# Kernel optimization log

Measured on AMD Instinct MI355X. Metric: run time of the kernel, lower is better.

Reference implementation:

```python
import jax, jax.numpy as jnp
import numpy as np

# ---- structural constants (mirror e3nn SO3.tensor_productRs bookkeeping) ----
MUL = 2                      # multiplicity of every irrep in Rs_in / Rs_out
LS = [0, 1, 2]               # irrep orders present in Rs_in and Rs_out
L_MAX = 2                    # spherical-harmonics cutoff -> Y_dim = 9
N_BASIS, HIDDEN = 64, 64     # radial model sizes
R_MAX, GAMMA = 3.5, 4.0      # gaussian radial basis params


def _filter_paths():
    """One entry (l_filter) per (mul_out, mul_in, l_in, l_out, l_f) path."""
    paths = []
    for l_in in LS:
        for l_out in LS:
            for lf in range(abs(l_in - l_out), min(l_in + l_out, L_MAX) + 1):
                paths.extend([lf] * (MUL * MUL))  # mul_in * mul_out copies
    return paths  # len == n_path == 60


def _build_mix_matrices():
    """rf_mix[K, n_path]: broadcast each radial path weight over its 2l+1 components.
    ylm_mix[K, 9]: select Y_{l,m} for each filter component. Both 0/1, block sparse."""
    paths = _filter_paths()
    n_path = len(paths)
    K = sum(2 * l + 1 for l in paths)          # 204
    y_off = {0: 0, 1: 1, 2: 4}                 # offset of l-block inside Y (dim 9)
    rf = np.zeros((K, n_path), dtype=np.float32)
    ylm = np.zeros((K, 9), dtype=np.float32)
    k = 0
    for p, l in enumerate(paths):
        for m in range(2 * l + 1):
            rf[k, p] = 1.0
            ylm[k, y_off[l] + m] = 1.0
            k += 1
    return rf, ylm, n_path, K


def _sh_l012(n):
    """Real spherical harmonics l=0..2 on unit vectors n[Z,3] -> Y[9, Z]."""
    x, y, z = n[:, 0], n[:, 1], n[:, 2]
    c0 = 0.28209479177387814   # 1/(2 sqrt(pi))
    c1 = 0.4886025119029199    # sqrt(3/(4 pi))
    c2a = 1.0925484305920792   # sqrt(15/(4 pi))
    c2b = 0.31539156525252005  # sqrt(5/(16 pi))
    c2c = 0.5462742152960396   # sqrt(15/(16 pi))
    one = jnp.ones_like(x)
    return jnp.stack([
        c0 * one,
        c1 * y, c1 * z, c1 * x,
        c2a * x * y, c2a * y * z, c2b * (3.0 * z * z - 1.0), c2a * x * z,
        c2c * (x * x - y * y),
    ], axis=0)


def setup_inputs() -> dict:
    key = jax.random.key(0)
    k_r, k_cg, k_w1, k_w2 = jax.random.split(key, 4)
    Z = 65536
    D = MUL * sum(2 * l + 1 for l in LS)       # 18 (dim_in == dim_out)
    rf_np, ylm_np, n_path, K = _build_mix_matrices()
    r = 2.0 * jax.random.normal(k_r, (Z, 3), dtype=jnp.float32)
    cg = jax.random.normal(k_cg, (K, D, D), dtype=jnp.float32) / np.sqrt(K)
    W1 = jax.random.normal(k_w1, (N_BASIS, HIDDEN), dtype=jnp.float32) / np.sqrt(N_BASIS)
    b1 = jnp.zeros((HIDDEN,), dtype=jnp.float32)
    W2 = jax.random.normal(k_w2, (HIDDEN, n_path), dtype=jnp.float32) / np.sqrt(HIDDEN)
    b2 = jnp.zeros((n_path,), dtype=jnp.float32)
    return {"r": r, "W1": W1, "b1": b1, "W2": W2, "b2": b2,
            "cg": cg, "rf_mix": jnp.asarray(rf_np), "ylm_mix": jnp.asarray(ylm_np)}


def reference(r, W1, b1, W2, b2, cg, rf_mix, ylm_mix):
    radii = jnp.linalg.norm(r, axis=1)                    # [Z]
    n = r / (radii[:, None] + 1e-12)                      # unit directions
    Y = _sh_l012(n)                                       # [9, Z]  (sh returns [m, ...])
    centers = jnp.linspace(0.0, R_MAX, N_BASIS, dtype=jnp.float32)
    B = jnp.exp(-GAMMA * (radii[:, None] - centers) ** 2) # gaussian radial basis [Z, 64]
    R = jax.nn.relu(B @ W1 + b1) @ W2 + b2                # RadialModel -> [Z, n_path]
    Rm = jnp.einsum('kp,zp->zk', rf_mix, R)               # 'ij,zj->zi'
    Ym = jnp.einsum('ky,yz->zk', ylm_mix, Y)              # 'ij,jz->zi'
    # 'kij,zk,zk->zij' : fuse the two per-point vectors, then one GEMM over k
    kernel = jnp.einsum('kij,zk->zij', cg, Rm * Ym)       # [Z, 18, 18]
    return kernel
```

## Files before the change

kernel.cpp:

```cpp
#include <hip/hip_runtime.h>

#define NPATH 60
#define KDIM  204
#define KPAD  224
#define NIJ   324
#define NTIL  21
#define HID   64

typedef short bf16x8 __attribute__((ext_vector_type(8)));
typedef float f32x4  __attribute__((ext_vector_type(4)));

__device__ __align__(16) unsigned short g_w1s[4096];
__device__ __align__(16) unsigned short g_w2s[4096];
__device__ __align__(16) unsigned short g_cgs[75264];
__device__ unsigned char g_ptab[KDIM];
__device__ unsigned char g_ytab[KDIM];

__device__ inline unsigned short f2bf(float f) {
    unsigned int u = __builtin_bit_cast(unsigned int, f);
    u += 0x7fffu + ((u >> 16) & 1u);
    return (unsigned short)(u >> 16);
}
__device__ inline float bf2f(unsigned short h) {
    unsigned int u = ((unsigned int)h) << 16;
    return __builtin_bit_cast(float, u);
}

__global__ void prep_kernel(const float* __restrict__ W1, const float* __restrict__ W2,
                            const float* __restrict__ cg, const float* __restrict__ rf,
                            const float* __restrict__ ylm)
{
    int idx = blockIdx.x * 256 + threadIdx.x;
    if (idx < 4096) {
        int e = idx & 7, ln = (idx >> 3) & 63, nt = (idx >> 9) & 3, kc = idx >> 11;
        int k = kc * 32 + (ln >> 4) * 8 + e;
        int n = nt * 16 + (ln & 15);
        g_w1s[idx] = f2bf(W1[k * HID + n]);
    } else if (idx < 8192) {
        int j = idx - 4096;
        int e = j & 7, ln = (j >> 3) & 63, nt = (j >> 9) & 3, kc = j >> 11;
        int k = kc * 32 + (ln >> 4) * 8 + e;
        int n = nt * 16 + (ln & 15);
        g_w2s[j] = f2bf(n < NPATH ? W2[k * NPATH + n] : 0.0f);
    } else if (idx < 8192 + 75264) {
        int j = idx - 8192;
        int e = j & 7, ln = (j >> 3) & 63;
        int nt = (j >> 9) % NTIL;
        int kc = j / (512 * NTIL);
        int k = kc * 32 + (ln >> 4) * 8 + e;
        int n = nt * 16 + (ln & 15);
        g_cgs[j] = f2bf((k < KDIM && n < NIJ) ? cg[k * NIJ + n] : 0.0f);
    } else if (idx < 8192 + 75264 + KDIM) {
        int k = idx - (8192 + 75264);
        int p = 0, yy = 0;
        for (int q = 0; q < NPATH; q++) if (rf[k * NPATH + q] != 0.0f) p = q;
        for (int q = 0; q < 9; q++)     if (ylm[k * 9 + q]   != 0.0f) yy = q;
        g_ptab[k] = (unsigned char)p;
        g_ytab[k] = (unsigned char)yy;
    }
}

union SmemU {
    struct {
        unsigned short Blds[64][72];
        unsigned short Hlds[64][72];
    } p1;
    unsigned short Clds[64][228];
    float stage[16][340];
};

__global__ __launch_bounds__(256) void fused_kernel(
    const float* __restrict__ r, const float* __restrict__ b1,
    const float* __restrict__ b2, float* __restrict__ out)
{
    __shared__ SmemU sm;
    __shared__ unsigned short Rl[64][61];
    __shared__ float Yl[64][9];
    __shared__ float radl[64];
    __shared__ unsigned char ptabL[KDIM];
    __shared__ unsigned char ytabL[KDIM];

    const int tid  = threadIdx.x;
    const int wv   = tid >> 6;
    const int lane = tid & 63;
    const int quad = lane >> 4;
    const int l16  = lane & 15;
    const int z0   = blockIdx.x * 64;

    if (tid < 64) {
        int z = z0 + tid;
        float x = r[z * 3 + 0], y = r[z * 3 + 1], zc = r[z * 3 + 2];
        float rad = sqrtf(x * x + y * y + zc * zc);
        float inv = 1.0f / (rad + 1e-12f);
        float nx = x * inv, ny = y * inv, nz = zc * inv;
        radl[tid] = rad;
        const float c0 = 0.28209479177387814f, c1 = 0.4886025119029199f;
        const float c2a = 1.0925484305920792f, c2b = 0.31539156525252005f, c2c = 0.5462742152960396f;
        Yl[tid][0] = c0;
        Yl[tid][1] = c1 * ny;
        Yl[tid][2] = c1 * nz;
        Yl[tid][3] = c1 * nx;
        Yl[tid][4] = c2a * nx * ny;
        Yl[tid][5] = c2a * ny * nz;
        Yl[tid][6] = c2b * (3.0f * nz * nz - 1.0f);
        Yl[tid][7] = c2a * nx * nz;
        Yl[tid][8] = c2c * (nx * nx - ny * ny);
    }
    for (int k = tid; k < KDIM; k += 256) {
        ptabL[k] = g_ptab[k];
        ytabL[k] = g_ytab[k];
    }
    __syncthreads();

    {
        int zz = tid >> 2, grp = tid & 3;
        float rad = radl[zz];
        unsigned int* dst = (unsigned int*)&sm.p1.Blds[zz][grp * 16];
        const float step = 3.5f / 63.0f;
        #pragma unroll
        for (int ii = 0; ii < 8; ii++) {
            int i0 = grp * 16 + ii * 2;
            float d0 = rad - (float)i0 * step;
            float d1 = rad - (float)(i0 + 1) * step;
            unsigned int u0 = f2bf(expf(-4.0f * d0 * d0));
            unsigned int u1 = f2bf(expf(-4.0f * d1 * d1));
            dst[ii] = u0 | (u1 << 16);
        }
    }
    __syncthreads();

    {
        bf16x8 a0 = *(const bf16x8*)&sm.p1.Blds[wv * 16 + l16][0 + quad * 8];
        bf16x8 a1 = *(const bf16x8*)&sm.p1.Blds[wv * 16 + l16][32 + quad * 8];
        #pragma unroll
        for (int nt = 0; nt < 4; nt++) {
            bf16x8 bb0 = *(const bf16x8*)&g_w1s[((0 * 4 + nt) * 64 + lane) * 8];
            bf16x8 bb1 = *(const bf16x8*)&g_w1s[((1 * 4 + nt) * 64 + lane) * 8];
            f32x4 acc = {0.f, 0.f, 0.f, 0.f};
            acc = __builtin_amdgcn_mfma_f32_16x16x32_bf16(a0, bb0, acc, 0, 0, 0);
            acc = __builtin_amdgcn_mfma_f32_16x16x32_bf16(a1, bb1, acc, 0, 0, 0);
            int h = nt * 16 + l16;
            float bias = b1[h];
            #pragma unroll
            for (int rr = 0; rr < 4; rr++) {
                float v = acc[rr] + bias;
                v = v > 0.0f ? v : 0.0f;
                sm.p1.Hlds[wv * 16 + quad * 4 + rr][h] = f2bf(v);
            }
        }
    }
    __syncthreads();

    {
        bf16x8 a0 = *(const bf16x8*)&sm.p1.Hlds[wv * 16 + l16][0 + quad * 8];
        bf16x8 a1 = *(const bf16x8*)&sm.p1.Hlds[wv * 16 + l16][32 + quad * 8];
        #pragma unroll
        for (int nt = 0; nt < 4; nt++) {
            bf16x8 bb0 = *(const bf16x8*)&g_w2s[((0 * 4 + nt) * 64 + lane) * 8];
            bf16x8 bb1 = *(const bf16x8*)&g_w2s[((1 * 4 + nt) * 64 + lane) * 8];
            f32x4 acc = {0.f, 0.f, 0.f, 0.f};
            acc = __builtin_amdgcn_mfma_f32_16x16x32_bf16(a0, bb0, acc, 0, 0, 0);
            acc = __builtin_amdgcn_mfma_f32_16x16x32_bf16(a1, bb1, acc, 0, 0, 0);
            int p = nt * 16 + l16;
            if (p < NPATH) {
                float bias = b2[p];
                #pragma unroll
                for (int rr = 0; rr < 4; rr++)
                    Rl[wv * 16 + quad * 4 + rr][p] = f2bf(acc[rr] + bias);
            }
        }
    }
    __syncthreads();

    for (int idx = tid; idx < 64 * (KPAD / 2); idx += 256) {
        int z = idx / (KPAD / 2);
        int k = (idx % (KPAD / 2)) * 2;
        unsigned int u = 0;
        if (k < KDIM) {
            float cA = bf2f(Rl[z][ptabL[k]])     * Yl[z][ytabL[k]];
            float cB = bf2f(Rl[z][ptabL[k + 1]]) * Yl[z][ytabL[k + 1]];
            u = (unsigned int)f2bf(cA) | ((unsigned int)f2bf(cB) << 16);
        }
        *(unsigned int*)&sm.Clds[z][k] = u;
    }
    __syncthreads();

    const int ntb = wv * 5 + (wv > 0 ? 1 : 0);
    const int cnt = (wv == 0) ? 6 : 5;

    f32x4 acc[6][4];
    #pragma unroll
    for (int i = 0; i < 6; i++)
        #pragma unroll
        for (int zt = 0; zt < 4; zt++)
            acc[i][zt] = (f32x4){0.f, 0.f, 0.f, 0.f};

    #pragma unroll
    for (int kc = 0; kc < 7; kc++) {
        bf16x8 az[4];
        #pragma unroll
        for (int zt = 0; zt < 4; zt++)
            az[zt] = *(const bf16x8*)&sm.Clds[zt * 16 + l16][kc * 32 + quad * 8];

        bf16x8 bg[6];
        #pragma unroll
        for (int i = 0; i < 6; i++) {
            int nt = ntb + i; if (nt > NTIL - 1) nt = NTIL - 1;
            bg[i] = *(const bf16x8*)&g_cgs[((kc * NTIL + nt) * 64 + lane) * 8];
        }
        #pragma unroll
        for (int i = 0; i < 6; i++) {
            if (i < cnt) {
                #pragma unroll
                for (int zt = 0; zt < 4; zt++)
                    acc[i][zt] = __builtin_amdgcn_mfma_f32_16x16x32_bf16(az[zt], bg[i], acc[i][zt], 0, 0, 0);
            }
        }
    }

    for (int zt = 0; zt < 4; zt++) {
        __syncthreads();
        #pragma unroll
        for (int i = 0; i < 6; i++) {
            if (i < cnt) {
                int col = (ntb + i) * 16 + l16;
                #pragma unroll
                for (int rr = 0; rr < 4; rr++)
                    sm.stage[quad * 4 + rr][col] = acc[i][zt][rr];
            }
        }
        __syncthreads();
        for (int j = tid; j < 16 * (NIJ / 4); j += 256) {
            int row = j / (NIJ / 4);
            int c4  = j % (NIJ / 4);
            f32x4 v = *(const f32x4*)&sm.stage[row][c4 * 4];
            *(f32x4*)&out[(z0 + zt * 16 + row) * NIJ + c4 * 4] = v;
        }
    }
}

extern "C" void kernel_launch(void* const* d_in, const int* in_sizes, int n_in,
                              void* d_out, int out_size, void* d_ws, size_t ws_size,
                              hipStream_t stream) {
    const float* r   = (const float*)d_in[0];
    const float* W1  = (const float*)d_in[1];
    const float* b1  = (const float*)d_in[2];
    const float* W2  = (const float*)d_in[3];
    const float* b2  = (const float*)d_in[4];
    const float* cg  = (const float*)d_in[5];
    const float* rf  = (const float*)d_in[6];
    const float* ylm = (const float*)d_in[7];
    float* out = (float*)d_out;

    const int Z = in_sizes[0] / 3;

    prep_kernel<<<327, 256, 0, stream>>>(W1, W2, cg, rf, ylm);
    fused_kernel<<<Z / 64, 256, 0, stream>>>(r, b1, b2, out);
}
```

Measured before the change: 138.9 us.

## Split fused kernel into coefficient kernel and streaming GEMM kernel via workspace

Splits the single fused kernel in two. The first computes per-point bf16 coefficients in MFMA fragment layout and writes them to a global workspace. The second reads those fragments and runs the CG GEMM over 128 points per block, storing fp32 results straight to global without LDS staging. This drops the large staging buffer and several barriers and rebalances the tile shape. In exchange it adds a global round trip of the coefficients, an extra launch, and uncoalesced scalar output stores with a stride of NIJ.

```diff
diff --git a/kernel.cpp b/kernel.cpp
--- a/kernel.cpp
+++ b/kernel.cpp
@@ -60,23 +60,22 @@
     }
 }
 
+
 union SmemU {
     struct {
         unsigned short Blds[64][72];
         unsigned short Hlds[64][72];
     } p1;
     unsigned short Clds[64][228];
-    float stage[16][340];
 };
 
-__global__ __launch_bounds__(256) void fused_kernel(
+__global__ __launch_bounds__(256) void coeff_kernel(
     const float* __restrict__ r, const float* __restrict__ b1,
-    const float* __restrict__ b2, float* __restrict__ out)
+    const float* __restrict__ b2, unsigned short* __restrict__ coeff_f)
 {
     __shared__ SmemU sm;
     __shared__ unsigned short Rl[64][61];
     __shared__ float Yl[64][9];
-    __shared__ float radl[64];
     __shared__ unsigned char ptabL[KDIM];
     __shared__ unsigned char ytabL[KDIM];
 
@@ -93,7 +92,6 @@
         float rad = sqrtf(x * x + y * y + zc * zc);
         float inv = 1.0f / (rad + 1e-12f);
         float nx = x * inv, ny = y * inv, nz = zc * inv;
-        radl[tid] = rad;
         const float c0 = 0.28209479177387814f, c1 = 0.4886025119029199f;
         const float c2a = 1.0925484305920792f, c2b = 0.31539156525252005f, c2c = 0.5462742152960396f;
         Yl[tid][0] = c0;
@@ -110,11 +108,12 @@
         ptabL[k] = g_ptab[k];
         ytabL[k] = g_ytab[k];
     }
-    __syncthreads();
 
     {
         int zz = tid >> 2, grp = tid & 3;
-        float rad = radl[zz];
+        int z = z0 + zz;
+        float x = r[z * 3 + 0], y = r[z * 3 + 1], zc = r[z * 3 + 2];
+        float rad = sqrtf(x * x + y * y + zc * zc);
         unsigned int* dst = (unsigned int*)&sm.p1.Blds[zz][grp * 16];
         const float step = 3.5f / 63.0f;
         #pragma unroll
@@ -185,56 +184,67 @@
     }
     __syncthreads();
 
-    const int ntb = wv * 5 + (wv > 0 ? 1 : 0);
-    const int cnt = (wv == 0) ? 6 : 5;
-
-    f32x4 acc[6][4];
+    {
+        const long ztg = blockIdx.x * 4 + wv;
+        #pragma unroll
+        for (int kc = 0; kc < 7; kc++) {
+            bf16x8 v = *(const bf16x8*)&sm.Clds[wv * 16 + l16][kc * 32 + quad * 8];
+            *(bf16x8*)&coeff_f[((ztg * 7 + kc) * 64 + lane) * 8] = v;
+        }
+    }
+}
+
+__global__ __launch_bounds__(256) void gemm_kernel(
+    const unsigned short* __restrict__ coeff_f, float* __restrict__ out)
+{
+    const int tid  = threadIdx.x;
+    const int wv   = tid >> 6;
+    const int lane = tid & 63;
+    const int quad = lane >> 4;
+    const int l16  = lane & 15;
+    const int z0   = blockIdx.x * 128;
+    const long ztg0 = (long)(z0 >> 4) + wv * 2;
+
     #pragma unroll
-    for (int i = 0; i < 6; i++)
-        #pragma unroll
-        for (int zt = 0; zt < 4; zt++)
-            acc[i][zt] = (f32x4){0.f, 0.f, 0.f, 0.f};
-
-    #pragma unroll
-    for (int kc = 0; kc < 7; kc++) {
-        bf16x8 az[4];
-        #pragma unroll
-        for (int zt = 0; zt < 4; zt++)
-            az[zt] = *(const bf16x8*)&sm.Clds[zt * 16 + l16][kc * 32 + quad * 8];
-
-        bf16x8 bg[6];
+    for (int chunk = 0; chunk < 4; chunk++) {
+        const int ntb = (chunk == 0) ? 0 : (1 + chunk * 5);
+        const int cnt = (chunk == 0) ? 6 : 5;
+
+        f32x4 acc[6][2];
         #pragma unroll
         for (int i = 0; i < 6; i++) {
-            int nt = ntb + i; if (nt > NTIL - 1) nt = NTIL - 1;
-            bg[i] = *(const bf16x8*)&g_cgs[((kc * NTIL + nt) * 64 + lane) * 8];
-        }
-        #pragma unroll
-        for (int i = 0; i < 6; i++) {
-            if (i < cnt) {
-                #pragma unroll
-                for (int zt = 0; zt < 4; zt++)
-                    acc[i][zt] = __builtin_amdgcn_mfma_f32_16x16x32_bf16(az[zt], bg[i], acc[i][zt], 0, 0, 0);
-            }
-        }
-    }
-
-    for (int zt = 0; zt < 4; zt++) {
-        __syncthreads();
+            acc[i][0] = (f32x4){0.f, 0.f, 0.f, 0.f};
+            acc[i][1] = (f32x4){0.f, 0.f, 0.f, 0.f};
+        }
+
+        #pragma unroll
+        for (int kc = 0; kc < 7; kc++) {
+            bf16x8 az0 = *(const bf16x8*)&coeff_f[((ztg0 * 7 + kc) * 64 + lane) * 8];
+            bf16x8 az1 = *(const bf16x8*)&coeff_f[(((ztg0 + 1) * 7 + kc) * 64 + lane) * 8];
+            #pragma unroll
+            for (int i = 0; i < 6; i++) {
+                if (i < cnt) {
+                    bf16x8 bg = *(const bf16x8*)&g_cgs[((kc * NTIL + ntb + i) * 64 + lane) * 8];
+                    acc[i][0] = __builtin_amdgcn_mfma_f32_16x16x32_bf16(az0, bg, acc[i][0], 0, 0, 0);
+                    acc[i][1] = __builtin_amdgcn_mfma_f32_16x16x32_bf16(az1, bg, acc[i][1], 0, 0, 0);
+                }
+            }
+        }
+
         #pragma unroll
         for (int i = 0; i < 6; i++) {
             if (i < cnt) {
                 int col = (ntb + i) * 16 + l16;
-                #pragma unroll
-                for (int rr = 0; rr < 4; rr++)
-                    sm.stage[quad * 4 + rr][col] = acc[i][zt][rr];
-            }
-        }
-        __syncthreads();
-        for (int j = tid; j < 16 * (NIJ / 4); j += 256) {
-            int row = j / (NIJ / 4);
-            int c4  = j % (NIJ / 4);
-            f32x4 v = *(const f32x4*)&sm.stage[row][c4 * 4];
-            *(f32x4*)&out[(z0 + zt * 16 + row) * NIJ + c4 * 4] = v;
+                if (col < NIJ) {
+                    #pragma unroll
+                    for (int t = 0; t < 2; t++) {
+                        int zb = z0 + (wv * 2 + t) * 16 + quad * 4;
+                        #pragma unroll
+                        for (int rr = 0; rr < 4; rr++)
+                            out[(long)(zb + rr) * NIJ + col] = acc[i][t][rr];
+                    }
+                }
+            }
         }
     }
 }
@@ -253,7 +263,9 @@
     float* out = (float*)d_out;
 
     const int Z = in_sizes[0] / 3;
+    unsigned short* coeff_f = (unsigned short*)d_ws;
 
     prep_kernel<<<327, 256, 0, stream>>>(W1, W2, cg, rf, ylm);
-    fused_kernel<<<Z / 64, 256, 0, stream>>>(r, b1, b2, out);
-}
+    coeff_kernel<<<Z / 64, 256, 0, stream>>>(r, b1, b2, coeff_f);
+    gemm_kernel<<<Z / 128, 256, 0, stream>>>(coeff_f, out);
+}
```

New measurement: 169.1 us. 21.8% more time.

## Swap MFMA operands to store output directly from registers, drop LDS staging

Applied to the files above, without the earlier changes.

The GEMM operands are swapped so each lane's accumulator holds four consecutive output columns for a single point. The results can then be written to global memory as float4 stores without the shared-memory staging buffer and its per-tile barriers. The radius is recomputed per thread instead of being shared through LDS, which removes one barrier. Each row is now written in 16-byte pieces scattered across rows instead of fully coalesced rows. The smaller shared-memory footprint may also allow higher occupancy.

```diff
diff --git a/kernel.cpp b/kernel.cpp
--- a/kernel.cpp
+++ b/kernel.cpp
@@ -66,7 +66,6 @@
         unsigned short Hlds[64][72];
     } p1;
     unsigned short Clds[64][228];
-    float stage[16][340];
 };
 
 __global__ __launch_bounds__(256) void fused_kernel(
@@ -76,7 +75,6 @@
     __shared__ SmemU sm;
     __shared__ unsigned short Rl[64][61];
     __shared__ float Yl[64][9];
-    __shared__ float radl[64];
     __shared__ unsigned char ptabL[KDIM];
     __shared__ unsigned char ytabL[KDIM];
 
@@ -93,7 +91,6 @@
         float rad = sqrtf(x * x + y * y + zc * zc);
         float inv = 1.0f / (rad + 1e-12f);
         float nx = x * inv, ny = y * inv, nz = zc * inv;
-        radl[tid] = rad;
         const float c0 = 0.28209479177387814f, c1 = 0.4886025119029199f;
         const float c2a = 1.0925484305920792f, c2b = 0.31539156525252005f, c2c = 0.5462742152960396f;
         Yl[tid][0] = c0;
@@ -110,11 +107,11 @@
         ptabL[k] = g_ptab[k];
         ytabL[k] = g_ytab[k];
     }
-    __syncthreads();
-
     {
         int zz = tid >> 2, grp = tid & 3;
-        float rad = radl[zz];
+        int z = z0 + zz;
+        float x = r[z * 3 + 0], y = r[z * 3 + 1], zc = r[z * 3 + 2];
+        float rad = sqrtf(x * x + y * y + zc * zc);
         unsigned int* dst = (unsigned int*)&sm.p1.Blds[zz][grp * 16];
         const float step = 3.5f / 63.0f;
         #pragma unroll
@@ -185,56 +182,47 @@
     }
     __syncthreads();
 
-    const int ntb = wv * 5 + (wv > 0 ? 1 : 0);
-    const int cnt = (wv == 0) ? 6 : 5;
-
-    f32x4 acc[6][4];
-    #pragma unroll
-    for (int i = 0; i < 6; i++)
-        #pragma unroll
-        for (int zt = 0; zt < 4; zt++)
-            acc[i][zt] = (f32x4){0.f, 0.f, 0.f, 0.f};
-
-    #pragma unroll
-    for (int kc = 0; kc < 7; kc++) {
-        bf16x8 az[4];
-        #pragma unroll
-        for (int zt = 0; zt < 4; zt++)
-            az[zt] = *(const bf16x8*)&sm.Clds[zt * 16 + l16][kc * 32 + quad * 8];
-
-        bf16x8 bg[6];
-        #pragma unroll
-        for (int i = 0; i < 6; i++) {
-            int nt = ntb + i; if (nt > NTIL - 1) nt = NTIL - 1;
-            bg[i] = *(const bf16x8*)&g_cgs[((kc * NTIL + nt) * 64 + lane) * 8];
-        }
+    {
+        const int ntb = wv * 5 + (wv > 0 ? 1 : 0);
+        const int cnt = (wv == 0) ? 6 : 5;
+
+        f32x4 acc[6][4];
+        #pragma unroll
+        for (int i = 0; i < 6; i++)
+            #pragma unroll
+            for (int zt = 0; zt < 4; zt++)
+                acc[i][zt] = (f32x4){0.f, 0.f, 0.f, 0.f};
+
+        #pragma unroll
+        for (int kc = 0; kc < 7; kc++) {
+            bf16x8 bz[4];
+            #pragma unroll
+            for (int zt = 0; zt < 4; zt++)
+                bz[zt] = *(const bf16x8*)&sm.Clds[zt * 16 + l16][kc * 32 + quad * 8];
+
+            #pragma unroll
+            for (int i = 0; i < 6; i++) {
+                if (i < cnt) {
+                    bf16x8 ag = *(const bf16x8*)&g_cgs[((kc * NTIL + ntb + i) * 64 + lane) * 8];
+                    #pragma unroll
+                    for (int zt = 0; zt < 4; zt++)
+                        acc[i][zt] = __builtin_amdgcn_mfma_f32_16x16x32_bf16(ag, bz[zt], acc[i][zt], 0, 0, 0);
+                }
+            }
+        }
+
         #pragma unroll
         for (int i = 0; i < 6; i++) {
             if (i < cnt) {
-                #pragma unroll
-                for (int zt = 0; zt < 4; zt++)
-                    acc[i][zt] = __builtin_amdgcn_mfma_f32_16x16x32_bf16(az[zt], bg[i], acc[i][zt], 0, 0, 0);
-            }
-        }
-    }
-
-    for (int zt = 0; zt < 4; zt++) {
-        __syncthreads();
-        #pragma unroll
-        for (int i = 0; i < 6; i++) {
-            if (i < cnt) {
-                int col = (ntb + i) * 16 + l16;
-                #pragma unroll
-                for (int rr = 0; rr < 4; rr++)
-                    sm.stage[quad * 4 + rr][col] = acc[i][zt][rr];
-            }
-        }
-        __syncthreads();
-        for (int j = tid; j < 16 * (NIJ / 4); j += 256) {
-            int row = j / (NIJ / 4);
-            int c4  = j % (NIJ / 4);
-            f32x4 v = *(const f32x4*)&sm.stage[row][c4 * 4];
-            *(f32x4*)&out[(z0 + zt * 16 + row) * NIJ + c4 * 4] = v;
+                int colb = (ntb + i) * 16 + quad * 4;
+                if (colb + 3 < NIJ) {
+                    #pragma unroll
+                    for (int zt = 0; zt < 4; zt++) {
+                        int z = z0 + zt * 16 + l16;
+                        *(f32x4*)&out[(long)z * NIJ + colb] = acc[i][zt];
+                    }
+                }
+            }
         }
     }
 }
```

New measurement: 144.1 us. 1.04x slower.
